# Optimization experiments

Hardware: AMD Instinct MI355X
Metric: run time of the kernel (lower is better)

The kernel has to match this reference:

```python
import jax, jax.numpy as jnp
import numpy as np

B, H, V, DEPTH = 64, 1024, 32000, 5


def setup_inputs() -> dict:
    key = jax.random.key(0)
    ks = jax.random.split(key, 9)
    s = 1.0 / np.sqrt(H)
    u = lambda k, shape: jax.random.uniform(k, shape, jnp.float32, -s, s)
    return {
        "encoding": jax.random.normal(ks[0], (B, H), jnp.float32),
        "Whh_l": u(ks[1], (3 * H, H)),
        "bih_l": u(ks[2], (3 * H,)),
        "bhh_l": u(ks[3], (3 * H,)),
        "Whh_r": u(ks[4], (3 * H, H)),
        "bih_r": u(ks[5], (3 * H,)),
        "bhh_r": u(ks[6], (3 * H,)),
        "W_out": u(ks[7], (V, H)),
        "b_out": u(ks[8], (V,)),
        "depth": DEPTH,
    }


def _gru_zero_input(h, Whh, bih, bhh):
    # PyTorch GRU cell with x == 0: W_ih @ x vanishes, only b_ih survives.
    d = h.shape[-1]
    gh = h @ Whh.T + bhh                                   # [N, 3H]
    r = jax.nn.sigmoid(bih[:d] + gh[..., :d])
    z = jax.nn.sigmoid(bih[d:2 * d] + gh[..., d:2 * d])
    n = jnp.tanh(bih[2 * d:] + r * gh[..., 2 * d:])
    return (1.0 - z) * n + z * h


def reference(encoding, Whh_l, bih_l, bhh_l, Whh_r, bih_r, bhh_r, W_out, b_out, depth):
    b, h = encoding.shape
    cur = encoding[:, None, :]                             # [B, 1, H] roots
    for _ in range(depth):                                 # expand perfect binary tree, level-batched
        n = cur.shape[1]
        flat = cur.reshape(b * n, h)
        left = _gru_zero_input(flat, Whh_l, bih_l, bhh_l).reshape(b, n, h)
        right = _gru_zero_input(flat, Whh_r, bih_r, bhh_r).reshape(b, n, h)
        cur = jnp.stack([left, right], axis=2).reshape(b, 2 * n, h)  # interleave children
    logits = jnp.einsum("blh,vh->blv", cur, W_out) + b_out  # [B, L, V]
    return jax.nn.log_softmax(logits, axis=-1)
```

## Files before the change

### kernel.cpp

```cpp
#include <hip/hip_runtime.h>
#include <hip/hip_bf16.h>
#include <cstdint>
#include <cstddef>

#define H_DIM   1024
#define B_DIM   64
#define V_DIM   32000
#define DEPTH_C 5

using bf16x8  = __attribute__((ext_vector_type(8))) __bf16;
using bf16x4  = __attribute__((ext_vector_type(4))) __bf16;
using floatx4 = __attribute__((ext_vector_type(4))) float;

__device__ __forceinline__ void gl_lds16(const __bf16* g, __bf16* l) {
  __builtin_amdgcn_global_load_lds(
      (const __attribute__((address_space(1))) unsigned int*)g,
      (__attribute__((address_space(3))) unsigned int*)l, 16, 0, 0);
}

__global__ __launch_bounds__(256) void f2b(const float* __restrict__ in,
                                           __bf16* __restrict__ out, int n) {
  for (int i = (blockIdx.x * 256 + threadIdx.x) * 4; i < n;
       i += gridDim.x * 1024) {
    float4 v = *(const float4*)(in + i);
    bf16x4 o;
    o[0] = (__bf16)v.x; o[1] = (__bf16)v.y; o[2] = (__bf16)v.z; o[3] = (__bf16)v.w;
    *(bf16x4*)(out + i) = o;
  }
}

__device__ __forceinline__ bf16x8 cvt8(float4 a, float4 b) {
  bf16x8 r;
  r[0] = (__bf16)a.x; r[1] = (__bf16)a.y; r[2] = (__bf16)a.z; r[3] = (__bf16)a.w;
  r[4] = (__bf16)b.x; r[5] = (__bf16)b.y; r[6] = (__bf16)b.z; r[7] = (__bf16)b.w;
  return r;
}

#define VMCNT(n) asm volatile("s_waitcnt vmcnt(" #n ")" ::: "memory")
#define SBAR()                                  \
  do {                                          \
    __builtin_amdgcn_sched_barrier(0);          \
    __builtin_amdgcn_s_barrier();               \
    __builtin_amdgcn_sched_barrier(0);          \
  } while (0)
#define LDA(MH, KS)                                                          \
  do {                                                                       \
    _Pragma("unroll") for (int mf = 0; mf < 4; ++mf)                         \
        aF[mf] = *(const bf16x8*)(cb + aRow + (MH)*8192 + mf * 2048 +        \
                                  ((KS) ? cksw1 : cksw0));                   \
  } while (0)
#define LDB(KS)                                                              \
  do {                                                                       \
    _Pragma("unroll") for (int nj = 0; nj < 4; ++nj)                         \
        bB[nj] = *(const bf16x8*)(cb + 32768 + bRow + nj * 2048 +            \
                                  ((KS) ? cksw1 : cksw0));                   \
  } while (0)
#define MM(MH)                                                               \
  do {                                                                       \
    __builtin_amdgcn_s_setprio(1);                                           \
    _Pragma("unroll") for (int mf = 0; mf < 4; ++mf)                         \
        _Pragma("unroll") for (int nj = 0; nj < 4; ++nj)                     \
            acc[(MH)*4 + mf][nj] = __builtin_amdgcn_mfma_f32_16x16x32_bf16(  \
                aF[mf], bB[nj], acc[(MH)*4 + mf][nj], 0, 0, 0);              \
    __builtin_amdgcn_s_setprio(0);                                           \
  } while (0)

__global__ __launch_bounds__(512, 2) void gemm_logits_8ph(
    const __bf16* __restrict__ A, const __bf16* __restrict__ Wb,
    float* __restrict__ Cf, const float* __restrict__ bias,
    float2* __restrict__ part) {
  __shared__ __align__(16) char smem[131072];

  const int tid = threadIdx.x;
  int h = blockIdx.y * 8 + blockIdx.x;
  h = (h & 7) * 125 + (h >> 3);
  const int bx = h & 7, by = h >> 3;
  const int m0 = bx * 256, n0 = by * 256;

  const int lane = tid & 63, wave = tid >> 6;
  const int wr = wave >> 2, wc = wave & 3;
  const int lrow = lane & 15, quad = lane >> 4;

  const int aRow  = (wr * 128 + lrow) * 128;
  const int bRow  = (wc * 64 + lrow) * 128;
  const int lsw   = (lrow & 7) << 4;
  const int cksw0 = (quad * 16) ^ lsw;
  const int cksw1 = (64 + quad * 16) ^ lsw;

  const int t8  = tid >> 3;
  const int cix = (tid & 7) ^ (t8 & 7);
  const __bf16* gA00 = A + (size_t)(m0 + t8) * 1024 + cix * 8;
  const __bf16* gA01 = A + (size_t)(m0 + 128 + t8) * 1024 + cix * 8;
  const __bf16* gA10 = gA00 + 64 * 1024;
  const __bf16* gA11 = gA01 + 64 * 1024;
  const __bf16* gB00 = Wb + (size_t)(n0 + t8) * 1024 + cix * 8;
  const __bf16* gB01 = Wb + (size_t)(n0 + 64 + t8) * 1024 + cix * 8;
  const __bf16* gB10 = gB00 + 128 * 1024;
  const __bf16* gB11 = gB01 + 128 * 1024;

  floatx4 acc[8][4] = {};
  bf16x8 aF[4], bB[4];

  gl_lds16(gA00, (__bf16*)(smem + tid * 16));
  gl_lds16(gA01, (__bf16*)(smem + 16384 + tid * 16));
  gl_lds16(gB00, (__bf16*)(smem + 32768 + tid * 16));
  gl_lds16(gB01, (__bf16*)(smem + 40960 + tid * 16));
  gl_lds16(gB10, (__bf16*)(smem + 49152 + tid * 16));
  gl_lds16(gB11, (__bf16*)(smem + 57344 + tid * 16));
  gl_lds16(gA10, (__bf16*)(smem + 8192 + tid * 16));
  gl_lds16(gA11, (__bf16*)(smem + 24576 + tid * 16));

  for (int t = 0; t < 15; ++t) {
    char* cb = smem + (t & 1) * 65536;
    char* nb = smem + ((t & 1) ^ 1) * 65536;
    const int ke = (t + 1) * 64;
    VMCNT(2); SBAR();
    LDB(0); LDA(0, 0);
    gl_lds16(gA00 + ke, (__bf16*)(nb + tid * 16));
    gl_lds16(gA01 + ke, (__bf16*)(nb + 16384 + tid * 16));
    MM(0);
    VMCNT(2); SBAR();
    LDA(1, 0);
    gl_lds16(gB00 + ke, (__bf16*)(nb + 32768 + tid * 16));
    gl_lds16(gB01 + ke, (__bf16*)(nb + 40960 + tid * 16));
    MM(1);
    LDB(1); LDA(0, 1);
    gl_lds16(gB10 + ke, (__bf16*)(nb + 49152 + tid * 16));
    gl_lds16(gB11 + ke, (__bf16*)(nb + 57344 + tid * 16));
    MM(0);
    LDA(1, 1);
    gl_lds16(gA10 + ke, (__bf16*)(nb + 8192 + tid * 16));
    gl_lds16(gA11 + ke, (__bf16*)(nb + 24576 + tid * 16));
    MM(1);
  }
  {
    char* cb = smem + 65536;
    VMCNT(0); SBAR();
    LDB(0); LDA(0, 0); MM(0);
    LDA(1, 0); MM(1);
    LDB(1); LDA(0, 1); MM(0);
    LDA(1, 1); MM(1);
  }

  float bv[4];
#pragma unroll
  for (int nj = 0; nj < 4; ++nj) bv[nj] = bias[n0 + wc * 64 + nj * 16 + lrow];

  float* pm = (float*)smem;
  float* ps = (float*)(smem + 4096);

#pragma unroll
  for (int mi = 0; mi < 8; ++mi) {
    const int rowb = wr * 128 + mi * 16 + quad * 4;
#pragma unroll
    for (int r = 0; r < 4; ++r) {
      const float v0 = acc[mi][0][r] + bv[0];
      const float v1 = acc[mi][1][r] + bv[1];
      const float v2 = acc[mi][2][r] + bv[2];
      const float v3 = acc[mi][3][r] + bv[3];
      const size_t rb = (size_t)(m0 + rowb + r) * V_DIM + n0 + wc * 64 + lrow;
      Cf[rb]      = v0;
      Cf[rb + 16] = v1;
      Cf[rb + 32] = v2;
      Cf[rb + 48] = v3;
      float mx = fmaxf(fmaxf(v0, v1), fmaxf(v2, v3));
#pragma unroll
      for (int msk = 1; msk < 16; msk <<= 1)
        mx = fmaxf(mx, __shfl_xor(mx, msk, 64));
      float sm = __expf(v0 - mx) + __expf(v1 - mx) + __expf(v2 - mx) +
                 __expf(v3 - mx);
#pragma unroll
      for (int msk = 1; msk < 16; msk <<= 1) sm += __shfl_xor(sm, msk, 64);
      if (lrow == 0) {
        pm[(rowb + r) * 4 + wc] = mx;
        ps[(rowb + r) * 4 + wc] = sm;
      }
    }
  }
  __syncthreads();
  if (tid < 256) {
    float m = pm[tid * 4], s = ps[tid * 4];
#pragma unroll
    for (int w = 1; w < 4; ++w) {
      const float om = pm[tid * 4 + w], os = ps[tid * 4 + w];
      const float nm = fmaxf(m, om);
      s = s * __expf(m - nm) + os * __expf(om - nm);
      m = nm;
    }
    part[(size_t)(m0 + tid) * gridDim.y + by] = make_float2(m, s);
  }
}

template <int TN, bool LOGITS, bool WBF16>
__global__ __launch_bounds__(256) void gemm_nt(
    const __bf16* __restrict__ A, const __bf16* __restrict__ Wb0,
    const __bf16* __restrict__ Wb1, const float* __restrict__ Wf,
    __bf16* __restrict__ Cb, float* __restrict__ Cf,
    const float* __restrict__ bias, float2* __restrict__ part, int M, int N) {
  constexpr int K = H_DIM;
  constexpr int MI = (TN == 128) ? 4 : 2;
  __shared__ __align__(16) __bf16 As[128 * 32];
  __shared__ __align__(16) __bf16 Bs[TN * 32];

  const int tid  = threadIdx.x;
  const int nbx = gridDim.x;
  const int nwg = nbx * gridDim.y;
  int hflat = blockIdx.y * nbx + blockIdx.x;
  if ((nwg & 7) == 0) {
    const int cpx = nwg >> 3;
    hflat = (hflat & 7) * cpx + (hflat >> 3);
  }
  const int bx = hflat % nbx;
  const int by = hflat / nbx;
  const int m0   = bx * 128;
  const int n0   = by * TN;
  const int lane = tid & 63;
  const int wave = tid >> 6;
  const int lrow = lane & 15;
  const int quad = lane >> 4;
  const int wm   = (TN == 128) ? (wave >> 1) * 64 : wave * 32;
  const int wn   = (TN == 128) ? (wave & 1) * 64 : 0;

  const __bf16* Wb = Wb0;
  int nw0 = n0;
  if (!LOGITS && n0 >= 3072) { Wb = Wb1; nw0 = n0 - 3072; }

  const int sr = tid >> 2;
  const int sk = (tid & 3) * 8;

  int ra0 = m0 + sr;      if (ra0 >= M) ra0 = M - 1;
  int ra1 = m0 + sr + 64; if (ra1 >= M) ra1 = M - 1;
  const __bf16* ga0 = A + (size_t)ra0 * K + sk;
  const __bf16* ga1 = A + (size_t)ra1 * K + sk;
  const __bf16* gb0 = nullptr; const __bf16* gb1 = nullptr;
  const float* gf0 = nullptr; const float* gf1 = nullptr;
  if (WBF16) {
    gb0 = Wb + (size_t)(nw0 + sr) * K + sk;
    if (TN == 128) gb1 = Wb + (size_t)(nw0 + sr + 64) * K + sk;
  } else {
    gf0 = Wf + (size_t)(n0 + sr) * K + sk;
    gf1 = Wf + (size_t)(n0 + sr + 64) * K + sk;
  }

  floatx4 acc[MI][4] = {};

  for (int kt = 0; kt < K; kt += 32) {
    float4 w00, w01, w10, w11;
    if (!WBF16) {
      w00 = *(const float4*)(gf0 + kt);
      w01 = *(const float4*)(gf0 + kt + 4);
      w10 = *(const float4*)(gf1 + kt);
      w11 = *(const float4*)(gf1 + kt + 4);
    }
    __syncthreads();
    gl_lds16(ga0 + kt, As + tid * 8);
    gl_lds16(ga1 + kt, As + 2048 + tid * 8);
    if (WBF16) {
      gl_lds16(gb0 + kt, Bs + tid * 8);
      if (TN == 128) gl_lds16(gb1 + kt, Bs + 2048 + tid * 8);
    } else {
      *(bf16x8*)(&Bs[sr * 32 + sk])        = cvt8(w00, w01);
      *(bf16x8*)(&Bs[(sr + 64) * 32 + sk]) = cvt8(w10, w11);
    }
    __syncthreads();

    bf16x8 af[MI], bfr[4];
#pragma unroll
    for (int i = 0; i < MI; i++)
      af[i] = *(const bf16x8*)(&As[(wm + i * 16 + lrow) * 32 + quad * 8]);
#pragma unroll
    for (int j = 0; j < 4; j++)
      bfr[j] = *(const bf16x8*)(&Bs[(wn + j * 16 + lrow) * 32 + quad * 8]);
#pragma unroll
    for (int i = 0; i < MI; i++)
#pragma unroll
      for (int j = 0; j < 4; j++)
        acc[i][j] =
            __builtin_amdgcn_mfma_f32_16x16x32_bf16(af[i], bfr[j], acc[i][j], 0, 0, 0);
  }

  float bv[4];
  if constexpr (LOGITS) {
#pragma unroll
    for (int j = 0; j < 4; j++) bv[j] = bias[n0 + wn + j * 16 + lrow];
  }
#pragma unroll
  for (int i = 0; i < MI; i++) {
#pragma unroll
    for (int j = 0; j < 4; j++) {
      const int col = n0 + wn + j * 16 + lrow;
#pragma unroll
      for (int r = 0; r < 4; r++) {
        const int row = m0 + wm + i * 16 + quad * 4 + r;
        if (row < M) {
          if (LOGITS) Cf[(size_t)row * N + col] = acc[i][j][r] + bv[j];
          else        Cb[(size_t)row * N + col] = (__bf16)acc[i][j][r];
        }
      }
    }
  }

  if constexpr (LOGITS) {
    __shared__ float pmax[2][128], psum[2][128];
    const int wnh = wn >> 6;
#pragma unroll
    for (int i = 0; i < MI; i++) {
#pragma unroll
      for (int r = 0; r < 4; r++) {
        float mx = -3.0e38f;
#pragma unroll
        for (int j = 0; j < 4; j++) mx = fmaxf(mx, acc[i][j][r] + bv[j]);
#pragma unroll
        for (int mask = 1; mask < 16; mask <<= 1)
          mx = fmaxf(mx, __shfl_xor(mx, mask, 64));
        float sm = 0.f;
#pragma unroll
        for (int j = 0; j < 4; j++) sm += __expf(acc[i][j][r] + bv[j] - mx);
#pragma unroll
        for (int mask = 1; mask < 16; mask <<= 1)
          sm += __shfl_xor(sm, mask, 64);
        if (lrow == 0) {
          pmax[wnh][wm + i * 16 + quad * 4 + r] = mx;
          psum[wnh][wm + i * 16 + quad * 4 + r] = sm;
        }
      }
    }
    __syncthreads();
    if (tid < 128) {
      const float ma = pmax[0][tid], mb = pmax[1][tid];
      const float nm = fmaxf(ma, mb);
      const float ns = psum[0][tid] * __expf(ma - nm) +
                       psum[1][tid] * __expf(mb - nm);
      part[(size_t)(m0 + tid) * gridDim.y + by] = make_float2(nm, ns);
    }
  }
}

__global__ __launch_bounds__(256) void gru_gate(
    const __bf16* __restrict__ gh, const float* __restrict__ bih_l,
    const float* __restrict__ bhh_l, const float* __restrict__ bih_r,
    const float* __restrict__ bhh_r, const __bf16* __restrict__ hin,
    __bf16* __restrict__ hout, int n) {
  const int row = blockIdx.x;
  const int col = blockIdx.y * 256 + threadIdx.x;
  const int b = row / n, j = row - b * n;
  const size_t g6 = (size_t)row * 6144;
  const float hv = (float)hin[(size_t)row * H_DIM + col];
  const size_t obase = (size_t)(b * 2 * n + 2 * j) * H_DIM;

  {
    float gr = (float)gh[g6 + col] + bhh_l[col];
    float gz = (float)gh[g6 + 1024 + col] + bhh_l[1024 + col];
    float gn = (float)gh[g6 + 2048 + col] + bhh_l[2048 + col];
    float r = 1.f / (1.f + __expf(-(bih_l[col] + gr)));
    float z = 1.f / (1.f + __expf(-(bih_l[1024 + col] + gz)));
    float nn = tanhf(bih_l[2048 + col] + r * gn);
    hout[obase + col] = (__bf16)((1.f - z) * nn + z * hv);
  }
  {
    float gr = (float)gh[g6 + 3072 + col] + bhh_r[col];
    float gz = (float)gh[g6 + 4096 + col] + bhh_r[1024 + col];
    float gn = (float)gh[g6 + 5120 + col] + bhh_r[2048 + col];
    float r = 1.f / (1.f + __expf(-(bih_r[col] + gr)));
    float z = 1.f / (1.f + __expf(-(bih_r[1024 + col] + gz)));
    float nn = tanhf(bih_r[2048 + col] + r * gn);
    hout[obase + H_DIM + col] = (__bf16)((1.f - z) * nn + z * hv);
  }
}

__global__ __launch_bounds__(256) void lsm_finish(
    float* __restrict__ out, const float2* __restrict__ part, int nb) {
  const int row = blockIdx.x;
  const int tid = threadIdx.x;

  float m = -3.0e38f, s = 0.f;
  if (tid < nb) {
    const float2 p = part[(size_t)row * nb + tid];
    m = p.x; s = p.y;
  }
#pragma unroll
  for (int off = 32; off; off >>= 1) {
    float om = __shfl_xor(m, off, 64);
    float os = __shfl_xor(s, off, 64);
    float nm = fmaxf(m, om);
    s = s * __expf(m - nm) + os * __expf(om - nm);
    m = nm;
  }
  __shared__ float rm[4], rs[4];
  if ((tid & 63) == 0) { rm[tid >> 6] = m; rs[tid >> 6] = s; }
  __syncthreads();
  const float M4 = fmaxf(fmaxf(rm[0], rm[1]), fmaxf(rm[2], rm[3]));
  const float S4 = rs[0] * __expf(rm[0] - M4) + rs[1] * __expf(rm[1] - M4) +
                   rs[2] * __expf(rm[2] - M4) + rs[3] * __expf(rm[3] - M4);
  const float lg = M4 + __logf(S4);

  float4* p4 = (float4*)(out + (size_t)row * V_DIM);
  for (int i = tid; i < 8000; i += 256) {
    float4 v = p4[i];
    v.x -= lg; v.y -= lg; v.z -= lg; v.w -= lg;
    p4[i] = v;
  }
}

extern "C" void kernel_launch(void* const* d_in, const int* in_sizes, int n_in,
                              void* d_out, int out_size, void* d_ws,
                              size_t ws_size, hipStream_t stream) {
  const float* enc   = (const float*)d_in[0];
  const float* Whh_l = (const float*)d_in[1];
  const float* bih_l = (const float*)d_in[2];
  const float* bhh_l = (const float*)d_in[3];
  const float* Whh_r = (const float*)d_in[4];
  const float* bih_r = (const float*)d_in[5];
  const float* bhh_r = (const float*)d_in[6];
  const float* W_out = (const float*)d_in[7];
  const float* b_out = (const float*)d_in[8];
  float* out = (float*)d_out;

  char* ws = (char*)d_ws;
  __bf16* ghb    = (__bf16*)ws;
  __bf16* buf0   = (__bf16*)(ws + 12582912);
  __bf16* buf1   = (__bf16*)(ws + 16777216);
  __bf16* WhhB_l = (__bf16*)(ws + 20971520);
  __bf16* WhhB_r = WhhB_l + 3145728;
  __bf16* encB   = (__bf16*)(ws + 33554432);
  __bf16* WoutB  = (__bf16*)(ws + 33685504);
  float2* part   = (float2*)ghb;
  const bool big = ws_size >= (size_t)(33685504 + 65536000);

  f2b<<<256, 256, 0, stream>>>(Whh_l, WhhB_l, 3 * H_DIM * H_DIM);
  f2b<<<256, 256, 0, stream>>>(Whh_r, WhhB_r, 3 * H_DIM * H_DIM);
  f2b<<<64, 256, 0, stream>>>(enc, encB, B_DIM * H_DIM);
  if (big) f2b<<<1024, 256, 0, stream>>>(W_out, WoutB, V_DIM * H_DIM);

  const __bf16* cur = encB;
  __bf16* nxt = buf0;
  int n = 1;
  for (int d = 0; d < DEPTH_C; d++) {
    const int M = B_DIM * n;
    dim3 gg((M + 127) / 128, 6144 / 64);
    gemm_nt<64, false, true><<<gg, 256, 0, stream>>>(
        cur, WhhB_l, WhhB_r, nullptr, ghb, nullptr, nullptr, nullptr, M, 6144);
    gru_gate<<<dim3(M, 4), 256, 0, stream>>>(ghb, bih_l, bhh_l, bih_r, bhh_r,
                                             cur, nxt, n);
    cur = nxt;
    nxt = (nxt == buf0) ? buf1 : buf0;
    n *= 2;
  }

  if (big) {
    gemm_logits_8ph<<<dim3(8, 125), 512, 0, stream>>>(cur, WoutB, out, b_out,
                                                      part);
    lsm_finish<<<2048, 256, 0, stream>>>(out, part, 125);
  } else {
    dim3 gf(2048 / 128, V_DIM / 128);
    gemm_nt<128, true, false><<<gf, 256, 0, stream>>>(
        cur, nullptr, nullptr, W_out, nullptr, out, b_out, part, 2048, V_DIM);
    lsm_finish<<<2048, 256, 0, stream>>>(out, part, 250);
  }
}
```

Before: 736.6 us.

## Rework logits GEMM waits, add dedicated tree GEMM, vectorize GRU gate

Three separate changes land together. The logits GEMM main loop moves its vmcnt waits and barriers and adds explicit lgkmcnt(0) waits before each MFMA phase, and the epilogue's first LDS reads are issued before the final vmcnt wait. A new double-buffered MFMA kernel, gemm_tree, replaces the generic gemm_nt for the per-level GRU hidden GEMMs. The gru_gate kernel is vectorized to four columns per thread, with a single block per row. The intent is better load/compute overlap and fewer instructions, at the cost of extra waits that could serialize LDS reads and MFMAs.

After: 736.1 us (median of 2 runs). Within noise of the previous version (-0.1%).

```diff
diff --git a/kernel.cpp b/kernel.cpp
--- a/kernel.cpp
+++ b/kernel.cpp
@@ -37,6 +37,11 @@
 }
 
 #define VMCNT(n) asm volatile("s_waitcnt vmcnt(" #n ")" ::: "memory")
+#define LGK0()                                  \
+  do {                                          \
+    asm volatile("s_waitcnt lgkmcnt(0)" ::: "memory"); \
+    __builtin_amdgcn_sched_barrier(0);          \
+  } while (0)
 #define SBAR()                                  \
   do {                                          \
     __builtin_amdgcn_sched_barrier(0);          \
@@ -109,34 +114,42 @@
   gl_lds16(gB11, (__bf16*)(smem + 57344 + tid * 16));
   gl_lds16(gA10, (__bf16*)(smem + 8192 + tid * 16));
   gl_lds16(gA11, (__bf16*)(smem + 24576 + tid * 16));
+  VMCNT(2);
+  SBAR();
 
   for (int t = 0; t < 15; ++t) {
     char* cb = smem + (t & 1) * 65536;
     char* nb = smem + ((t & 1) ^ 1) * 65536;
     const int ke = (t + 1) * 64;
-    VMCNT(2); SBAR();
     LDB(0); LDA(0, 0);
     gl_lds16(gA00 + ke, (__bf16*)(nb + tid * 16));
     gl_lds16(gA01 + ke, (__bf16*)(nb + 16384 + tid * 16));
+    SBAR(); LGK0();
     MM(0);
     VMCNT(2); SBAR();
     LDA(1, 0);
     gl_lds16(gB00 + ke, (__bf16*)(nb + 32768 + tid * 16));
     gl_lds16(gB01 + ke, (__bf16*)(nb + 40960 + tid * 16));
+    SBAR(); LGK0();
     MM(1);
+    SBAR();
     LDB(1); LDA(0, 1);
     gl_lds16(gB10 + ke, (__bf16*)(nb + 49152 + tid * 16));
     gl_lds16(gB11 + ke, (__bf16*)(nb + 57344 + tid * 16));
+    SBAR(); LGK0();
     MM(0);
+    SBAR();
     LDA(1, 1);
     gl_lds16(gA10 + ke, (__bf16*)(nb + 8192 + tid * 16));
     gl_lds16(gA11 + ke, (__bf16*)(nb + 24576 + tid * 16));
+    SBAR(); LGK0();
     MM(1);
+    VMCNT(2); SBAR();
   }
   {
     char* cb = smem + 65536;
+    LDB(0); LDA(0, 0); MM(0);
     VMCNT(0); SBAR();
-    LDB(0); LDA(0, 0); MM(0);
     LDA(1, 0); MM(1);
     LDB(1); LDA(0, 1); MM(0);
     LDA(1, 1); MM(1);
@@ -188,6 +201,90 @@
       m = nm;
     }
     part[(size_t)(m0 + tid) * gridDim.y + by] = make_float2(m, s);
+  }
+}
+
+__global__ __launch_bounds__(256) void gemm_tree(
+    const __bf16* __restrict__ A, const __bf16* __restrict__ Wb0,
+    const __bf16* __restrict__ Wb1, __bf16* __restrict__ Cb, int M) {
+  constexpr int K = H_DIM;
+  __shared__ __align__(16) __bf16 As[2][128 * 32];
+  __shared__ __align__(16) __bf16 Bs[2][64 * 32];
+
+  const int tid = threadIdx.x;
+  const int nbx = gridDim.x;
+  const int nwg = nbx * gridDim.y;
+  int hflat = blockIdx.y * nbx + blockIdx.x;
+  if ((nwg & 7) == 0) {
+    const int cpx = nwg >> 3;
+    hflat = (hflat & 7) * cpx + (hflat >> 3);
+  }
+  const int bx = hflat % nbx;
+  const int by = hflat / nbx;
+  const int m0 = bx * 128;
+  const int n0 = by * 64;
+  const int lane = tid & 63, wave = tid >> 6;
+  const int lrow = lane & 15, quad = lane >> 4;
+  const int wm = wave * 32;
+
+  const __bf16* Wb = Wb0;
+  int nw0 = n0;
+  if (n0 >= 3072) { Wb = Wb1; nw0 = n0 - 3072; }
+
+  const int sr = tid >> 2;
+  const int sk = (tid & 3) * 8;
+  int ra0 = m0 + sr;      if (ra0 >= M) ra0 = M - 1;
+  int ra1 = m0 + sr + 64; if (ra1 >= M) ra1 = M - 1;
+  const __bf16* ga0 = A + (size_t)ra0 * K + sk;
+  const __bf16* ga1 = A + (size_t)ra1 * K + sk;
+  const __bf16* gb0 = Wb + (size_t)(nw0 + sr) * K + sk;
+
+  floatx4 acc[2][4] = {};
+
+  gl_lds16(ga0, As[0] + tid * 8);
+  gl_lds16(ga1, As[0] + 2048 + tid * 8);
+  gl_lds16(gb0, Bs[0] + tid * 8);
+  VMCNT(0);
+  __syncthreads();
+
+  int cur = 0;
+  for (int kt = 0; kt < K; kt += 32) {
+    if (kt + 32 < K) {
+      gl_lds16(ga0 + kt + 32, As[cur ^ 1] + tid * 8);
+      gl_lds16(ga1 + kt + 32, As[cur ^ 1] + 2048 + tid * 8);
+      gl_lds16(gb0 + kt + 32, Bs[cur ^ 1] + tid * 8);
+    }
+    bf16x8 af[2], bfr[4];
+#pragma unroll
+    for (int i = 0; i < 2; i++)
+      af[i] = *(const bf16x8*)(&As[cur][(wm + i * 16 + lrow) * 32 + quad * 8]);
+#pragma unroll
+    for (int j = 0; j < 4; j++)
+      bfr[j] = *(const bf16x8*)(&Bs[cur][(j * 16 + lrow) * 32 + quad * 8]);
+#pragma unroll
+    for (int i = 0; i < 2; i++)
+#pragma unroll
+      for (int j = 0; j < 4; j++)
+        acc[i][j] = __builtin_amdgcn_mfma_f32_16x16x32_bf16(af[i], bfr[j],
+                                                            acc[i][j], 0, 0, 0);
+    if (kt + 32 < K) {
+      VMCNT(0);
+      __syncthreads();
+      cur ^= 1;
+    }
+  }
+
+#pragma unroll
+  for (int i = 0; i < 2; i++) {
+#pragma unroll
+    for (int j = 0; j < 4; j++) {
+      const int col = n0 + j * 16 + lrow;
+#pragma unroll
+      for (int r = 0; r < 4; r++) {
+        const int row = m0 + wm + i * 16 + quad * 4 + r;
+        if (row < M) Cb[(size_t)row * 6144 + col] = (__bf16)acc[i][j][r];
+      }
+    }
   }
 }
 
@@ -342,30 +439,45 @@
     const float* __restrict__ bhh_r, const __bf16* __restrict__ hin,
     __bf16* __restrict__ hout, int n) {
   const int row = blockIdx.x;
-  const int col = blockIdx.y * 256 + threadIdx.x;
+  const int c = threadIdx.x * 4;
   const int b = row / n, j = row - b * n;
   const size_t g6 = (size_t)row * 6144;
-  const float hv = (float)hin[(size_t)row * H_DIM + col];
+  const bf16x4 h4 = *(const bf16x4*)(hin + (size_t)row * H_DIM + c);
   const size_t obase = (size_t)(b * 2 * n + 2 * j) * H_DIM;
 
-  {
-    float gr = (float)gh[g6 + col] + bhh_l[col];
-    float gz = (float)gh[g6 + 1024 + col] + bhh_l[1024 + col];
-    float gn = (float)gh[g6 + 2048 + col] + bhh_l[2048 + col];
-    float r = 1.f / (1.f + __expf(-(bih_l[col] + gr)));
-    float z = 1.f / (1.f + __expf(-(bih_l[1024 + col] + gz)));
-    float nn = tanhf(bih_l[2048 + col] + r * gn);
-    hout[obase + col] = (__bf16)((1.f - z) * nn + z * hv);
-  }
-  {
-    float gr = (float)gh[g6 + 3072 + col] + bhh_r[col];
-    float gz = (float)gh[g6 + 4096 + col] + bhh_r[1024 + col];
-    float gn = (float)gh[g6 + 5120 + col] + bhh_r[2048 + col];
-    float r = 1.f / (1.f + __expf(-(bih_r[col] + gr)));
-    float z = 1.f / (1.f + __expf(-(bih_r[1024 + col] + gz)));
-    float nn = tanhf(bih_r[2048 + col] + r * gn);
-    hout[obase + H_DIM + col] = (__bf16)((1.f - z) * nn + z * hv);
-  }
+  bf16x4 og[2];
+#pragma unroll
+  for (int side = 0; side < 2; ++side) {
+    const float* bih = side ? bih_r : bih_l;
+    const float* bhh = side ? bhh_r : bhh_l;
+    const size_t gb = g6 + side * 3072;
+    const bf16x4 g0 = *(const bf16x4*)(gh + gb + c);
+    const bf16x4 g1 = *(const bf16x4*)(gh + gb + 1024 + c);
+    const bf16x4 g2 = *(const bf16x4*)(gh + gb + 2048 + c);
+    const float4 br0 = *(const float4*)(bih + c);
+    const float4 br1 = *(const float4*)(bih + 1024 + c);
+    const float4 br2 = *(const float4*)(bih + 2048 + c);
+    const float4 bh0 = *(const float4*)(bhh + c);
+    const float4 bh1 = *(const float4*)(bhh + 1024 + c);
+    const float4 bh2 = *(const float4*)(bhh + 2048 + c);
+    const float* pr0 = (const float*)&br0; const float* ph0 = (const float*)&bh0;
+    const float* pr1 = (const float*)&br1; const float* ph1 = (const float*)&bh1;
+    const float* pr2 = (const float*)&br2; const float* ph2 = (const float*)&bh2;
+    bf16x4 o;
+#pragma unroll
+    for (int e = 0; e < 4; ++e) {
+      const float gr = (float)g0[e] + ph0[e];
+      const float gz = (float)g1[e] + ph1[e];
+      const float gn = (float)g2[e] + ph2[e];
+      const float r = 1.f / (1.f + __expf(-(pr0[e] + gr)));
+      const float z = 1.f / (1.f + __expf(-(pr1[e] + gz)));
+      const float nn = tanhf(pr2[e] + r * gn);
+      o[e] = (__bf16)((1.f - z) * nn + z * (float)h4[e]);
+    }
+    og[side] = o;
+  }
+  *(bf16x4*)(hout + obase + c) = og[0];
+  *(bf16x4*)(hout + obase + H_DIM + c) = og[1];
 }
 
 __global__ __launch_bounds__(256) void lsm_finish(
@@ -438,10 +550,9 @@
   for (int d = 0; d < DEPTH_C; d++) {
     const int M = B_DIM * n;
     dim3 gg((M + 127) / 128, 6144 / 64);
-    gemm_nt<64, false, true><<<gg, 256, 0, stream>>>(
-        cur, WhhB_l, WhhB_r, nullptr, ghb, nullptr, nullptr, nullptr, M, 6144);
-    gru_gate<<<dim3(M, 4), 256, 0, stream>>>(ghb, bih_l, bhh_l, bih_r, bhh_r,
-                                             cur, nxt, n);
+    gemm_tree<<<gg, 256, 0, stream>>>(cur, WhhB_l, WhhB_r, ghb, M);
+    gru_gate<<<dim3(M), 256, 0, stream>>>(ghb, bih_l, bhh_l, bih_r, bhh_r,
+                                          cur, nxt, n);
     cur = nxt;
     nxt = (nxt == buf0) ? buf1 : buf0;
     n *= 2;
```
